# Kernel optimization log

Measured on AMD Instinct MI355X. Metric: run time of the kernel, lower is better.

Reference implementation:

```python
import jax, jax.numpy as jnp
import numpy as np

B, T, D, K = 32, 1024, 256, 1024


def setup_inputs() -> dict:
    key = jax.random.key(0)
    k1, k2 = jax.random.split(key)
    x = jax.random.normal(k1, (B, T, D), dtype=jnp.float32)
    # nn.Embedding init: uniform(-1/emb_size, 1/emb_size)
    embedding = jax.random.uniform(k2, (K, D), dtype=jnp.float32,
                                   minval=-1.0 / K, maxval=1.0 / K)
    return {"x": x, "embedding": embedding}


def reference(x, embedding):
    # x: [B, T, D], embedding: [K, D]
    Bx, Tx, Dx = x.shape
    flat = x.reshape(-1, Dx)  # [N, D]
    dist = (jnp.sum(embedding * embedding, axis=1)
            - 2.0 * flat @ embedding.T
            + jnp.sum(flat * flat, axis=1, keepdims=True))
    quantized_idx = jnp.argmin(dist, axis=1).reshape(Bx, Tx)  # [B, T] int
    # onehot @ W  ==  gather rows of W
    embed_idx = embedding[quantized_idx]  # [B, T, D]
    # straight-through estimator
    embed_idx_qx = x + jax.lax.stop_gradient(embed_idx - x)
    return embed_idx, embed_idx_qx, quantized_idx
```

## Files before the change

kernel.cpp:

```cpp
#include <hip/hip_runtime.h>
#include <math.h>

#define N_ROWS 32768
#define DIM    256
#define KCODES 1024
#define DELTA  5.0e-4f

typedef float f32x4 __attribute__((ext_vector_type(4)));
typedef short s16x8 __attribute__((ext_vector_type(8)));

__device__ inline unsigned short bf_rne(float f) {
    unsigned u = __float_as_uint(f);
    return (unsigned short)((u + 0x7FFFu + ((u >> 16) & 1u)) >> 16);
}

__device__ inline void ins4(float v, int ix, float (&tv)[4], int (&ti)[4]) {
#pragma unroll
    for (int s = 0; s < 4; ++s) {
        bool better = (v < tv[s]) || (v == tv[s] && ix < ti[s]);
        float dv = better ? tv[s] : v;
        int   di = better ? ti[s] : ix;
        tv[s] = better ? v : tv[s];
        ti[s] = better ? ix : ti[s];
        v = dv; ix = di;
    }
}

__device__ __forceinline__ void gl_lds16(const void* gp, void* lp) {
    __builtin_amdgcn_global_load_lds(
        (__attribute__((address_space(1))) void*)(void*)gp,
        (__attribute__((address_space(3))) void*)lp, 16, 0, 0);
}

__global__ __launch_bounds__(256) void prep_kernel(const float* __restrict__ E,
                                                   float* __restrict__ e2,
                                                   unsigned short* __restrict__ Eh) {
    __shared__ float sq[4][260];
    const int wave = threadIdx.x >> 6;
    const int lane = threadIdx.x & 63;
    const int row = blockIdx.x * 4 + wave;
    const float4* rp = (const float4*)(E + (size_t)row * DIM);
    float4 v = rp[lane];
    sq[wave][lane * 4 + 0] = v.x * v.x;
    sq[wave][lane * 4 + 1] = v.y * v.y;
    sq[wave][lane * 4 + 2] = v.z * v.z;
    sq[wave][lane * 4 + 3] = v.w * v.w;
    float fs[4] = {v.x, v.y, v.z, v.w};
    ushort4 hv;
    unsigned short* hp = (unsigned short*)&hv;
#pragma unroll
    for (int j = 0; j < 4; ++j) hp[j] = bf_rne(fs[j]);
    *(ushort4*)(Eh + (size_t)row * DIM + lane * 4) = hv;
    if (lane < 8) {
#pragma clang fp contract(off)
        const int j = lane;
        float rA = sq[wave][j];
#pragma unroll
        for (int m = 1; m < 16; ++m) rA += sq[wave][8 * m + j];
        float rB = sq[wave][128 + j];
#pragma unroll
        for (int m = 1; m < 16; ++m) rB += sq[wave][128 + 8 * m + j];
        rA = rA + __shfl_xor(rA, 1, 64); rA = rA + __shfl_xor(rA, 2, 64);
        rA = rA + __shfl_xor(rA, 4, 64);
        rB = rB + __shfl_xor(rB, 1, 64); rB = rB + __shfl_xor(rB, 2, 64);
        rB = rB + __shfl_xor(rB, 4, 64);
        if (j == 0) e2[row] = rA + rB;
    }
}

__device__ float x2_exact(const float* __restrict__ xr) {
#pragma clang fp contract(off)
    float rr[16];
#pragma unroll
    for (int j = 0; j < 8; ++j) {
        float a = xr[j] * xr[j];
#pragma unroll
        for (int m = 1; m < 16; ++m) { float t = xr[8 * m + j]; float s = t * t; a += s; }
        rr[j] = a;
        float b = xr[128 + j] * xr[128 + j];
#pragma unroll
        for (int m = 1; m < 16; ++m) { float t = xr[128 + 8 * m + j]; float s = t * t; b += s; }
        rr[8 + j] = b;
    }
    float a01 = rr[0] + rr[1], a23 = rr[2] + rr[3];
    float a45 = rr[4] + rr[5], a67 = rr[6] + rr[7];
    float A = (a01 + a23) + (a45 + a67);
    float b01 = rr[8] + rr[9], b23 = rr[10] + rr[11];
    float b45 = rr[12] + rr[13], b67 = rr[14] + rr[15];
    float Bt = (b01 + b23) + (b45 + b67);
    return A + Bt;
}

__global__ __launch_bounds__(256) void vq_screen_kernel(const float* __restrict__ X,
                                                        const unsigned short* __restrict__ Eh,
                                                        const float* __restrict__ e2g,
                                                        float* __restrict__ topv,
                                                        int* __restrict__ topi) {
    __shared__ __align__(16) short buf[3][4096];
    __shared__ __align__(16) float e2_lds[KCODES];

    const int tid  = threadIdx.x;
    const int w    = tid >> 6;
    const int l    = tid & 63;
    const int c16  = l & 15;
    const int quad = l >> 4;
    const int row0 = blockIdx.x * 64;

    gl_lds16(e2g + w * 256 + l * 4, &e2_lds[w * 256]);

    s16x8 xh[8];
    {
        const float* xrow = X + (size_t)(row0 + w * 16 + c16) * DIM + quad * 8;
#pragma unroll
        for (int ks = 0; ks < 8; ++ks) {
            float4 f0 = *(const float4*)(xrow + ks * 32);
            float4 f1 = *(const float4*)(xrow + ks * 32 + 4);
            float fs[8] = {f0.x, f0.y, f0.z, f0.w, f1.x, f1.y, f1.z, f1.w};
#pragma unroll
            for (int j = 0; j < 8; ++j) xh[ks][j] = (short)bf_rne(fs[j]);
        }
    }

    auto stage = [&](int t) {
        const unsigned short* Ehc = Eh + (size_t)(t * 16 + c16) * DIM + quad * 8;
        short* bp = &buf[t % 3][0];
#pragma unroll
        for (int gg = 0; gg < 2; ++gg) {
            const int ks = w + gg * 4;
            gl_lds16(Ehc + ks * 32, bp + ks * 512);
        }
    };

    stage(0);
    stage(1);

    float tva[4];
    int   tia[4];
#pragma unroll
    for (int s = 0; s < 4; ++s) { tva[s] = INFINITY; tia[s] = 0x7fffffff; }

    for (int t = 0; t < 64; ++t) {
        asm volatile("s_waitcnt vmcnt(2)" ::: "memory");
        __builtin_amdgcn_s_barrier();
        __builtin_amdgcn_sched_barrier(0);
        if (t < 62) stage(t + 2);

        const short* bp = &buf[t % 3][0];
        s16x8 ch[8];
#pragma unroll
        for (int ks = 0; ks < 8; ++ks)
            ch[ks] = *(const s16x8*)(bp + ks * 512 + l * 8);

        f32x4 ce = {0.f, 0.f, 0.f, 0.f};
        f32x4 co = {0.f, 0.f, 0.f, 0.f};
#pragma unroll
        for (int ks = 0; ks < 8; ks += 2) {
            ce = __builtin_amdgcn_mfma_f32_16x16x32_bf16(ch[ks],     xh[ks],     ce, 0, 0, 0);
            co = __builtin_amdgcn_mfma_f32_16x16x32_bf16(ch[ks + 1], xh[ks + 1], co, 0, 0, 0);
        }
        f32x4 e2v = *(const f32x4*)&e2_lds[t * 16 + quad * 4];
#pragma unroll
        for (int r = 0; r < 4; ++r) {
            const int code = t * 16 + quad * 4 + r;
            ins4(fmaf(-2.0f, ce[r] + co[r], e2v[r]), code, tva, tia);
        }
    }

#pragma unroll
    for (int st = 16; st <= 32; st <<= 1) {
        float ov[4]; int oi[4];
#pragma unroll
        for (int s = 0; s < 4; ++s) {
            ov[s] = __shfl_xor(tva[s], st, 64);
            oi[s] = __shfl_xor(tia[s], st, 64);
        }
#pragma unroll
        for (int s = 0; s < 4; ++s) ins4(ov[s], oi[s], tva, tia);
    }

    if (quad == 0) {
        const int r = row0 + w * 16 + c16;
#pragma unroll
        for (int s = 0; s < 4; ++s) {
            topv[r * 4 + s] = tva[s];
            topi[r * 4 + s] = tia[s];
        }
    }
}

__global__ __launch_bounds__(256) void decide_gather_kernel(const float* __restrict__ X,
                                                            const float* __restrict__ E,
                                                            const float* __restrict__ e2g,
                                                            const float* __restrict__ topv,
                                                            const int* __restrict__ topi,
                                                            float* __restrict__ out0,
                                                            float* __restrict__ out1,
                                                            float* __restrict__ out2) {
    __shared__ int sidx[64];
    const int tid  = threadIdx.x;
    const int row0 = blockIdx.x * 64;
    if (tid < 64) {
        const int r = row0 + tid;
        float tv[4]; int ti[4];
#pragma unroll
        for (int s = 0; s < 4; ++s) { tv[s] = topv[r * 4 + s]; ti[s] = topi[r * 4 + s]; }

        int best = ti[0];
        if (!(tv[1] > tv[0] + DELTA)) {
            const float* xr = X + (size_t)r * DIM;
            const float x2v = x2_exact(xr);
            float bq = INFINITY; int bi = 0x7fffffff;
            for (int cnd = 0; cnd < 4; ++cnd) {
                if (tv[cnd] <= tv[0] + DELTA) {
                    const int k = ti[cnd];
                    const float* er = E + (size_t)k * DIM;
                    float dot = 0.f;
                    for (int d = 0; d < DIM; d += 4) {
                        float4 xv = *(const float4*)(xr + d);
                        float4 ev = *(const float4*)(er + d);
                        dot = fmaf(xv.x, ev.x, dot);
                        dot = fmaf(xv.y, ev.y, dot);
                        dot = fmaf(xv.z, ev.z, dot);
                        dot = fmaf(xv.w, ev.w, dot);
                    }
                    float t1 = e2g[k] - 2.0f * dot;
                    float q  = t1 + x2v;
                    if (q < bq || (q == bq && k < bi)) { bq = q; bi = k; }
                }
            }
            best = bi;
        }
        sidx[tid] = best;
        out2[r] = (float)best;
    }
    __syncthreads();
#pragma unroll
    for (int it = 0; it < 16; ++it) {
        int f = tid + it * 256;
        int rr = f >> 6;
        int pp = f & 63;
        int ix = sidx[rr];
        float4 v = *(const float4*)(E + (size_t)ix * DIM + pp * 4);
        size_t o = (size_t)(row0 + rr) * DIM + (size_t)pp * 4;
        *(float4*)(out0 + o) = v;
        *(float4*)(out1 + o) = v;
    }
}

extern "C" void kernel_launch(void* const* d_in, const int* in_sizes, int n_in,
                              void* d_out, int out_size, void* d_ws, size_t ws_size,
                              hipStream_t stream) {
    const float* X = (const float*)d_in[0];
    const float* E = (const float*)d_in[1];

    float* e2 = (float*)d_ws;
    unsigned short* Eh = (unsigned short*)(e2 + KCODES);
    float* topv = (float*)(Eh + KCODES * DIM);
    int*   topi = (int*)(topv + N_ROWS * 4);

    float* out0 = (float*)d_out;
    float* out1 = out0 + (size_t)N_ROWS * DIM;
    float* out2 = out1 + (size_t)N_ROWS * DIM;

    prep_kernel<<<dim3(KCODES / 4), dim3(256), 0, stream>>>(E, e2, Eh);
    vq_screen_kernel<<<dim3(N_ROWS / 64), dim3(256), 0, stream>>>(X, Eh, e2,
                                                                  topv, topi);
    decide_gather_kernel<<<dim3(N_ROWS / 64), dim3(256), 0, stream>>>(X, E, e2,
                                                                      topv, topi,
                                                                      out0, out1, out2);
}
```

Before: 198.6 us.

## Split codebook search across blocks and merge per-split top-4 in decide kernel

The screening kernel now splits the 1024 codes into four ranges, each handled by its own block, so there are four times as many blocks, each running a shorter loop. Each block writes its own top-4 candidates, and the decide kernel merges the four partial lists. Code tile order is rotated per row block to spread L2 traffic, and indices are stored as 16-bit values to cut workspace bandwidth. The cost is that each block repeats the X load and bf16 conversion, and partial-result traffic goes up four times.

```diff
diff --git a/kernel.cpp b/kernel.cpp
--- a/kernel.cpp
+++ b/kernel.cpp
@@ -5,6 +5,8 @@
 #define DIM    256
 #define KCODES 1024
 #define DELTA  5.0e-4f
+#define CSPLIT 4
+#define TILES  (KCODES / 16 / CSPLIT)
 
 typedef float f32x4 __attribute__((ext_vector_type(4)));
 typedef short s16x8 __attribute__((ext_vector_type(8)));
@@ -95,18 +97,22 @@
                                                         const unsigned short* __restrict__ Eh,
                                                         const float* __restrict__ e2g,
                                                         float* __restrict__ topv,
-                                                        int* __restrict__ topi) {
+                                                        unsigned short* __restrict__ topi) {
     __shared__ __align__(16) short buf[3][4096];
-    __shared__ __align__(16) float e2_lds[KCODES];
+    __shared__ __align__(16) float e2_lds[256];
 
     const int tid  = threadIdx.x;
     const int w    = tid >> 6;
     const int l    = tid & 63;
     const int c16  = l & 15;
     const int quad = l >> 4;
-    const int row0 = blockIdx.x * 64;
-
-    gl_lds16(e2g + w * 256 + l * 4, &e2_lds[w * 256]);
+    const int bx   = blockIdx.x;
+    const int h    = bx & (CSPLIT - 1);
+    const int rb   = bx >> 2;
+    const int row0 = rb * 64;
+    const int cbase = h * (KCODES / CSPLIT);
+
+    if (w == 0) gl_lds16(e2g + cbase + l * 4, &e2_lds[0]);
 
     s16x8 xh[8];
     {
@@ -121,8 +127,11 @@
         }
     }
 
+    const int rot = rb & (TILES - 1);
     auto stage = [&](int t) {
-        const unsigned short* Ehc = Eh + (size_t)(t * 16 + c16) * DIM + quad * 8;
+        const int ct = (t + rot) & (TILES - 1);
+        const unsigned short* Ehc =
+            Eh + (size_t)(cbase + ct * 16 + c16) * DIM + quad * 8;
         short* bp = &buf[t % 3][0];
 #pragma unroll
         for (int gg = 0; gg < 2; ++gg) {
@@ -139,12 +148,13 @@
 #pragma unroll
     for (int s = 0; s < 4; ++s) { tva[s] = INFINITY; tia[s] = 0x7fffffff; }
 
-    for (int t = 0; t < 64; ++t) {
+    for (int t = 0; t < TILES; ++t) {
         asm volatile("s_waitcnt vmcnt(2)" ::: "memory");
         __builtin_amdgcn_s_barrier();
         __builtin_amdgcn_sched_barrier(0);
-        if (t < 62) stage(t + 2);
-
+        if (t < TILES - 2) stage(t + 2);
+
+        const int ct = (t + rot) & (TILES - 1);
         const short* bp = &buf[t % 3][0];
         s16x8 ch[8];
 #pragma unroll
@@ -158,10 +168,10 @@
             ce = __builtin_amdgcn_mfma_f32_16x16x32_bf16(ch[ks],     xh[ks],     ce, 0, 0, 0);
             co = __builtin_amdgcn_mfma_f32_16x16x32_bf16(ch[ks + 1], xh[ks + 1], co, 0, 0, 0);
         }
-        f32x4 e2v = *(const f32x4*)&e2_lds[t * 16 + quad * 4];
+        f32x4 e2v = *(const f32x4*)&e2_lds[ct * 16 + quad * 4];
 #pragma unroll
         for (int r = 0; r < 4; ++r) {
-            const int code = t * 16 + quad * 4 + r;
+            const int code = cbase + ct * 16 + quad * 4 + r;
             ins4(fmaf(-2.0f, ce[r] + co[r], e2v[r]), code, tva, tia);
         }
     }
@@ -180,10 +190,11 @@
 
     if (quad == 0) {
         const int r = row0 + w * 16 + c16;
+        const size_t o = ((size_t)h * N_ROWS + r) * 4;
 #pragma unroll
         for (int s = 0; s < 4; ++s) {
-            topv[r * 4 + s] = tva[s];
-            topi[r * 4 + s] = tia[s];
+            topv[o + s] = tva[s];
+            topi[o + s] = (unsigned short)tia[s];
         }
     }
 }
@@ -192,7 +203,7 @@
                                                             const float* __restrict__ E,
                                                             const float* __restrict__ e2g,
                                                             const float* __restrict__ topv,
-                                                            const int* __restrict__ topi,
+                                                            const unsigned short* __restrict__ topi,
                                                             float* __restrict__ out0,
                                                             float* __restrict__ out1,
                                                             float* __restrict__ out2) {
@@ -203,7 +214,13 @@
         const int r = row0 + tid;
         float tv[4]; int ti[4];
 #pragma unroll
-        for (int s = 0; s < 4; ++s) { tv[s] = topv[r * 4 + s]; ti[s] = topi[r * 4 + s]; }
+        for (int s = 0; s < 4; ++s) { tv[s] = INFINITY; ti[s] = 0x7fffffff; }
+#pragma unroll
+        for (int hh = 0; hh < CSPLIT; ++hh) {
+            const size_t o = ((size_t)hh * N_ROWS + r) * 4;
+#pragma unroll
+            for (int s = 0; s < 4; ++s) ins4(topv[o + s], (int)topi[o + s], tv, ti);
+        }
 
         int best = ti[0];
         if (!(tv[1] > tv[0] + DELTA)) {
@@ -256,15 +273,16 @@
     float* e2 = (float*)d_ws;
     unsigned short* Eh = (unsigned short*)(e2 + KCODES);
     float* topv = (float*)(Eh + KCODES * DIM);
-    int*   topi = (int*)(topv + N_ROWS * 4);
+    unsigned short* topi =
+        (unsigned short*)(topv + (size_t)CSPLIT * N_ROWS * 4);
 
     float* out0 = (float*)d_out;
     float* out1 = out0 + (size_t)N_ROWS * DIM;
     float* out2 = out1 + (size_t)N_ROWS * DIM;
 
     prep_kernel<<<dim3(KCODES / 4), dim3(256), 0, stream>>>(E, e2, Eh);
-    vq_screen_kernel<<<dim3(N_ROWS / 64), dim3(256), 0, stream>>>(X, Eh, e2,
-                                                                  topv, topi);
+    vq_screen_kernel<<<dim3((N_ROWS / 64) * CSPLIT), dim3(256), 0, stream>>>(X, Eh, e2,
+                                                                             topv, topi);
     decide_gather_kernel<<<dim3(N_ROWS / 64), dim3(256), 0, stream>>>(X, E, e2,
                                                                       topv, topi,
                                                                       out0, out1, out2);
```

After: 193.1 us. 2.8% less time.
